# Kernel tuning notes

Measured on AMD Instinct MI355X. Metric: run time of the kernel, lower is better.

## Reference

```python
import jax, jax.numpy as jnp
import numpy as np

B, C, H, W = 16, 256, 64, 64
NUM_HEADS = 4
GROUPS = 8
EPS = 1e-5


def setup_inputs() -> dict:
    key = jax.random.key(0)
    ks = jax.random.split(key, 7)
    x = jax.random.normal(ks[0], (B, C, H, W), dtype=jnp.float32)
    # GroupNorm affine params (torch default: weight=1, bias=0; randomize slightly for a stronger test)
    norm_w = jnp.ones((C,), jnp.float32) + 0.1 * jax.random.normal(ks[1], (C,), jnp.float32)
    norm_b = 0.1 * jax.random.normal(ks[2], (C,), jnp.float32)
    # 1x1 convs == channel GEMMs; kaiming-uniform-ish init scale
    s = 1.0 / np.sqrt(C)
    qkv_w = jax.random.uniform(ks[3], (3 * C, C), jnp.float32, -s, s)
    qkv_b = jax.random.uniform(ks[4], (3 * C,), jnp.float32, -s, s)
    proj_w = jax.random.uniform(ks[5], (C, C), jnp.float32, -s, s)
    proj_b = jax.random.uniform(ks[6], (C,), jnp.float32, -s, s)
    return {"x": x, "norm_w": norm_w, "norm_b": norm_b,
            "qkv_w": qkv_w, "qkv_b": qkv_b, "proj_w": proj_w, "proj_b": proj_b}


def reference(x, norm_w, norm_b, qkv_w, qkv_b, proj_w, proj_b):
    b, c, h, w = x.shape
    nh = NUM_HEADS
    dh = c // nh
    n = h * w
    # GroupNorm(8, C)
    xg = x.reshape(b, GROUPS, c // GROUPS, h, w)
    mean = xg.mean(axis=(2, 3, 4), keepdims=True)
    var = xg.var(axis=(2, 3, 4), keepdims=True)
    xn = ((xg - mean) * jax.lax.rsqrt(var + EPS)).reshape(b, c, h, w)
    xn = xn * norm_w[None, :, None, None] + norm_b[None, :, None, None]
    # QKV 1x1 conv as channel GEMM
    qkv = jnp.einsum('bchw,oc->bohw', xn, qkv_w) + qkv_b[None, :, None, None]
    qkv = qkv.reshape(b, 3, nh, dh, n)
    q, k, v = qkv[:, 0], qkv[:, 1], qkv[:, 2]  # each (B, nh, dh, N)
    scale = dh ** (-0.5)
    # Faithful to original einsum labeling: contracts over spatial axis,
    # attention matrix is over the HEADS axis: attn (B, dh, nh, nh)
    attn = jnp.einsum('bnhd,bmhd->bhnm', q * scale, k)
    attn = jax.nn.softmax(attn, axis=-1)
    out = jnp.einsum('bhnm,bmhd->bnhd', attn, v).reshape(b, c, h, w)
    return jnp.einsum('bchw,oc->bohw', out, proj_w) + proj_b[None, :, None, None] + x
```

## Files before the change

kernel.cpp:

```cpp
#include <hip/hip_runtime.h>
#include <stdint.h>

#define BB 16
#define CC 256
#define PP 4096

typedef __attribute__((ext_vector_type(4))) float f32x4;
typedef __attribute__((ext_vector_type(8))) short bf16x8;

static __device__ __forceinline__ float bf2f(unsigned short u) {
    union { uint32_t i; float f; } w; w.i = ((uint32_t)u) << 16; return w.f;
}
static __device__ __forceinline__ unsigned short f2bf(float f) {
    union { float f; uint32_t i; } w; w.f = f;
    uint32_t u = w.i;
    uint32_t r = u + 0x7FFFu + ((u >> 16) & 1u);
    return (unsigned short)(r >> 16);
}
static __device__ __forceinline__ float dot4(f32x4 a, f32x4 b) {
    return a.x * b.x + a.y * b.y + a.z * b.z + a.w * b.w;
}

__global__ void gn_partial_k(const float* __restrict__ x, float* __restrict__ Sx,
                             float* __restrict__ Sxx) {
    int ch0 = blockIdx.x * 8;
    int t = threadIdx.x;
    int lc = t >> 5, l32 = t & 31;
    int ch = ch0 + lc;
    const f32x4* v = (const f32x4*)(x + (size_t)ch * PP);
    float s = 0.f, ss = 0.f;
    for (int i = l32; i < PP / 4; i += 32) {
        f32x4 tv = v[i];
        s  += tv.x + tv.y + tv.z + tv.w;
        ss += tv.x * tv.x + tv.y * tv.y + tv.z * tv.z + tv.w * tv.w;
    }
    for (int off = 16; off > 0; off >>= 1) {
        s  += __shfl_down(s, off, 32);
        ss += __shfl_down(ss, off, 32);
    }
    if (l32 == 0) { Sx[ch] = s; Sxx[ch] = ss; }
}

__global__ void gn_final_k(const float* __restrict__ Sx, const float* __restrict__ Sxx,
                           const float* __restrict__ nw, const float* __restrict__ nb,
                           float* __restrict__ a_s, float* __restrict__ b_s,
                           float* __restrict__ s_vec) {
    int b = blockIdx.x, c = threadIdx.x;
    __shared__ float lsx[256], lsxx[256];
    float mySx = Sx[b * CC + c];
    lsx[c] = mySx; lsxx[c] = Sxx[b * CC + c];
    __syncthreads();
    int g0 = (c >> 5) << 5;
    float S = 0.f, SS = 0.f;
    for (int j = 0; j < 32; j++) { S += lsx[g0 + j]; SS += lsxx[g0 + j]; }
    const float inv = 1.0f / 131072.0f;
    float mean = S * inv;
    float var = SS * inv - mean * mean;
    float rstd = rsqrtf(var + 1e-5f);
    float w = nw[c];
    float a = rstd * w;
    float sh = nb[c] - mean * rstd * w;
    a_s[b * CC + c] = a;
    b_s[b * CC + c] = sh;
    s_vec[b * CC + c] = a * mySx + 4096.0f * sh;
}

__global__ void cvt_bf16_k(const float* __restrict__ in, unsigned short* __restrict__ out, int n) {
    int i = blockIdx.x * 256 + threadIdx.x;
    if (i < n) out[i] = f2bf(in[i]);
}

__global__ void wvt_k(const float* __restrict__ Wv, unsigned short* __restrict__ WvT) {
    int tc1 = blockIdx.x & 3, tc2 = blockIdx.x >> 2;
    int c1_0 = tc1 * 64, c2_0 = tc2 * 64;
    __shared__ unsigned short T[64][65];
    int t = threadIdx.x;
    int r = t >> 2, q = (t & 3) * 16;
    for (int j = 0; j < 4; j++) {
        f32x4 v = *(const f32x4*)(Wv + (size_t)(c1_0 + r) * 256 + c2_0 + q + j * 4);
        T[r][q + j * 4 + 0] = f2bf(v.x);
        T[r][q + j * 4 + 1] = f2bf(v.y);
        T[r][q + j * 4 + 2] = f2bf(v.z);
        T[r][q + j * 4 + 3] = f2bf(v.w);
    }
    __syncthreads();
    union { unsigned short h[16]; uint4 u[2]; } buf;
    for (int j = 0; j < 16; j++) buf.h[j] = T[q + j][r];
    unsigned short* dst = WvT + (size_t)(c2_0 + r) * 256 + c1_0 + q;
    *(uint4*)dst       = buf.u[0];
    *(uint4*)(dst + 8) = buf.u[1];
}

__global__ void xnt_k(const float* __restrict__ x, const float* __restrict__ a_s,
                      const float* __restrict__ b_s, unsigned short* __restrict__ xnT,
                      unsigned short* __restrict__ xnC) {
    int pt = blockIdx.x & 63, ct = (blockIdx.x >> 6) & 3, b = blockIdx.x >> 8;
    int c0 = ct * 64, p0 = pt * 64;
    __shared__ unsigned short T[64][66];
    int t = threadIdx.x;
    int cl = t >> 4, pl4 = (t & 15) * 4;
    for (int i = 0; i < 4; i++) {
        int c = c0 + i * 16 + cl;
        float a = a_s[b * CC + c], sh = b_s[b * CC + c];
        f32x4 v = *(const f32x4*)(x + ((size_t)b * CC + c) * PP + p0 + pl4);
        ushort4 u;
        u.x = f2bf(a * v.x + sh);
        u.y = f2bf(a * v.y + sh);
        u.z = f2bf(a * v.z + sh);
        u.w = f2bf(a * v.w + sh);
        T[i * 16 + cl][pl4 + 0] = u.x;
        T[i * 16 + cl][pl4 + 1] = u.y;
        T[i * 16 + cl][pl4 + 2] = u.z;
        T[i * 16 + cl][pl4 + 3] = u.w;
        *(ushort4*)(xnC + ((size_t)b * CC + c) * PP + p0 + pl4) = u;
    }
    __syncthreads();
    int pl = t >> 2, c16 = (t & 3) * 16;
    union { unsigned short h[16]; uint4 u[2]; } buf;
    for (int j = 0; j < 16; j++) buf.h[j] = T[c16 + j][pl];
    unsigned short* dst = xnT + ((size_t)b * PP + p0 + pl) * CC + c0 + c16;
    *(uint4*)dst       = buf.u[0];
    *(uint4*)(dst + 8) = buf.u[1];
}

static __device__ __forceinline__ void gemm_core(const unsigned short* __restrict__ Rg,
                                                 const unsigned short* __restrict__ Cg,
                                                 int kLen, int rstride,
                                                 f32x4 (&acc)[4][4]) {
    __shared__ unsigned short Rs[128][32];
    __shared__ unsigned short Cs[128][32];
    int t = threadIdx.x;
    int lane = t & 63, wave = t >> 6;
    int wm = wave >> 1, wn = wave & 1;
    int lr = lane & 15, lq = lane >> 4;
    int srow = t >> 2;
    int ssl = ((t & 3) ^ ((t >> 3) & 3)) * 8;
    int sd  = (t & 3) * 8;
    int fsw = (lr >> 1) & 3;
    for (int mi = 0; mi < 4; mi++)
        for (int ni = 0; ni < 4; ni++) {
            acc[mi][ni][0] = 0.f; acc[mi][ni][1] = 0.f;
            acc[mi][ni][2] = 0.f; acc[mi][ni][3] = 0.f;
        }
    const unsigned short* gr0 = Rg + (size_t)srow * rstride + ssl;
    const unsigned short* gr1 = gr0 + (size_t)64 * rstride;
    const unsigned short* gc0 = Cg + (size_t)srow * rstride + ssl;
    const unsigned short* gc1 = gc0 + (size_t)64 * rstride;
    uint4 ra0 = *(const uint4*)(gr0);
    uint4 ra1 = *(const uint4*)(gr1);
    uint4 rc0 = *(const uint4*)(gc0);
    uint4 rc1 = *(const uint4*)(gc1);
    for (int k0 = 0; k0 < kLen; k0 += 32) {
        __syncthreads();
        *(uint4*)&Rs[srow][sd]      = ra0;
        *(uint4*)&Rs[srow + 64][sd] = ra1;
        *(uint4*)&Cs[srow][sd]      = rc0;
        *(uint4*)&Cs[srow + 64][sd] = rc1;
        __syncthreads();
        int kn = k0 + 32;
        if (kn < kLen) {
            ra0 = *(const uint4*)(gr0 + kn);
            ra1 = *(const uint4*)(gr1 + kn);
            rc0 = *(const uint4*)(gc0 + kn);
            rc1 = *(const uint4*)(gc1 + kn);
        }
        bf16x8 af[4], bfr[4];
        for (int mi = 0; mi < 4; mi++)
            af[mi]  = *(const bf16x8*)&Rs[wm * 64 + mi * 16 + lr][(lq ^ fsw) * 8];
        for (int ni = 0; ni < 4; ni++)
            bfr[ni] = *(const bf16x8*)&Cs[wn * 64 + ni * 16 + lr][(lq ^ fsw) * 8];
        for (int mi = 0; mi < 4; mi++)
            for (int ni = 0; ni < 4; ni++)
                acc[mi][ni] = __builtin_amdgcn_mfma_f32_16x16x32_bf16(af[mi], bfr[ni], acc[mi][ni], 0, 0, 0);
    }
}

__global__ __launch_bounds__(256, 3) void gram_k(const unsigned short* __restrict__ xnC,
                                                 float* __restrict__ Gpart) {
    int pc  = blockIdx.x & 7;
    int t12 = (blockIdx.x >> 3) & 3;
    int b   = blockIdx.x >> 5;
    int t1 = (t12 >> 1) * 128;
    int t2 = (t12 & 1) * 128;
    f32x4 acc[4][4];
    gemm_core(xnC + ((size_t)b * CC + t2) * PP + pc * 512,
              xnC + ((size_t)b * CC + t1) * PP + pc * 512, 512, PP, acc);
    int t = threadIdx.x, lane = t & 63, wave = t >> 6;
    int wm = wave >> 1, wn = wave & 1, lr = lane & 15, lq = lane >> 4;
    float* dst = Gpart + ((size_t)(pc * 16 + b)) * 65536;
    for (int mi = 0; mi < 4; mi++) {
        int c2q = t2 + wm * 64 + mi * 16 + lq * 4;
        for (int ni = 0; ni < 4; ni++) {
            int c1 = t1 + wn * 64 + ni * 16 + lr;
            *(f32x4*)(dst + (size_t)c1 * 256 + c2q) = acc[mi][ni];
        }
    }
}

__global__ void greduce_k(const float* __restrict__ Gpart, unsigned short* __restrict__ Gb) {
    int i = blockIdx.x * 256 + threadIdx.x;
    float s = 0.f;
    for (int pc = 0; pc < 8; pc++) s += Gpart[(size_t)pc * 16 * 65536 + i];
    Gb[i] = f2bf(s);
}

__global__ __launch_bounds__(256, 3) void u_gemm_k(const unsigned short* __restrict__ Gb,
                                                   const unsigned short* __restrict__ Wqkvb,
                                                   float* __restrict__ UT) {
    int t12 = blockIdx.x & 3, b = blockIdx.x >> 2;
    int t1 = (t12 >> 1) * 128;
    int t2 = (t12 & 1) * 128;
    f32x4 acc[4][4];
    gemm_core(Gb + ((size_t)b * 256 + t1) * 256,
              Wqkvb + (size_t)(256 + t2) * 256, 256, 256, acc);
    int t = threadIdx.x, lane = t & 63, wave = t >> 6;
    int wm = wave >> 1, wn = wave & 1, lr = lane & 15, lq = lane >> 4;
    for (int mi = 0; mi < 4; mi++) {
        int c1q = t1 + wm * 64 + mi * 16 + lq * 4;
        for (int ni = 0; ni < 4; ni++) {
            int kr = t2 + wn * 64 + ni * 16 + lr;
            *(f32x4*)(UT + ((size_t)b * 256 + kr) * 256 + c1q) = acc[mi][ni];
        }
    }
}

__global__ void scoresfin_k(const float* __restrict__ qkv_w, const float* __restrict__ qkv_b,
                            const float* __restrict__ UT, const float* __restrict__ s_vec,
                            float* __restrict__ attn) {
    int h = blockIdx.x & 63, b = blockIdx.x >> 6;
    int l = threadIdx.x;
    int c = l * 4;
    f32x4 sv = *(const f32x4*)(s_vec + b * CC + c);
    f32x4 wq[4], wk[4], ut[4];
    for (int n = 0; n < 4; n++) wq[n] = *(const f32x4*)(qkv_w + (size_t)(n * 64 + h) * 256 + c);
    for (int m = 0; m < 4; m++) wk[m] = *(const f32x4*)(qkv_w + (size_t)(256 + m * 64 + h) * 256 + c);
    for (int m = 0; m < 4; m++) ut[m] = *(const f32x4*)(UT + ((size_t)b * 256 + m * 64 + h) * 256 + c);
    float red[24];
    for (int n = 0; n < 4; n++)
        for (int m = 0; m < 4; m++) red[n * 4 + m] = dot4(wq[n], ut[m]);
    for (int n = 0; n < 4; n++) red[16 + n] = dot4(wq[n], sv);
    for (int m = 0; m < 4; m++) red[20 + m] = dot4(wk[m], sv);
    #pragma unroll
    for (int i = 0; i < 24; i++)
        for (int off = 32; off > 0; off >>= 1)
            red[i] += __shfl_xor(red[i], off);
    __shared__ float sred[24];
    if (l == 0)
        for (int i = 0; i < 24; i++) sred[i] = red[i];
    __syncthreads();
    if (l < 4) {
        int n = l;
        float bq = qkv_b[n * 64 + h];
        float dqn = sred[16 + n];
        float lg[4];
        for (int m = 0; m < 4; m++) {
            float bk = qkv_b[256 + m * 64 + h];
            lg[m] = 0.125f * (sred[n * 4 + m] + bq * sred[20 + m] + bk * dqn + 4096.0f * bq * bk);
        }
        float mx = fmaxf(fmaxf(lg[0], lg[1]), fmaxf(lg[2], lg[3]));
        float e0 = expf(lg[0] - mx), e1 = expf(lg[1] - mx);
        float e2 = expf(lg[2] - mx), e3 = expf(lg[3] - mx);
        float inv = 1.0f / (e0 + e1 + e2 + e3);
        float* dst = attn + ((size_t)(b * 64 + h) * 4 + n) * 4;
        dst[0] = e0 * inv; dst[1] = e1 * inv; dst[2] = e2 * inv; dst[3] = e3 * inv;
    }
}

__global__ void make_wp_k(const float* __restrict__ proj_w, const float* __restrict__ attn,
                          const float* __restrict__ qkv_b, const float* __restrict__ proj_b,
                          unsigned short* __restrict__ Wp, float* __restrict__ bias2) {
    int t = threadIdx.x;
    int o = blockIdx.x & 255, b = blockIdx.x >> 8;
    int m = t >> 6, hh = t & 63;
    float s = 0.f;
    for (int n = 0; n < 4; n++)
        s += proj_w[o * 256 + n * 64 + hh] * attn[((size_t)(b * 64 + hh) * 4 + n) * 4 + m];
    Wp[((size_t)b * 256 + o) * 256 + t] = f2bf(s);
    float contrib = s * qkv_b[512 + t];
    int lane = t & 63, wave = t >> 6;
    for (int off = 32; off > 0; off >>= 1) contrib += __shfl_down(contrib, off);
    __shared__ float red[4];
    if (lane == 0) red[wave] = contrib;
    __syncthreads();
    if (t == 0) bias2[b * 256 + o] = proj_b[o] + red[0] + red[1] + red[2] + red[3];
}

__global__ __launch_bounds__(256, 3) void make_wc_k(const unsigned short* __restrict__ WvT,
                                                    const unsigned short* __restrict__ Wp,
                                                    unsigned short* __restrict__ Wc) {
    int t12 = blockIdx.x & 3, b = blockIdx.x >> 2;
    int c20 = (t12 & 1) * 128;
    int o0  = (t12 >> 1) * 128;
    f32x4 acc[4][4];
    gemm_core(WvT + (size_t)c20 * 256, Wp + ((size_t)b * 256 + o0) * 256, 256, 256, acc);
    int t = threadIdx.x, lane = t & 63, wave = t >> 6;
    int wm = wave >> 1, wn = wave & 1, lr = lane & 15, lq = lane >> 4;
    for (int mi = 0; mi < 4; mi++) {
        int c2q = c20 + wm * 64 + mi * 16 + lq * 4;
        for (int ni = 0; ni < 4; ni++) {
            int o = o0 + wn * 64 + ni * 16 + lr;
            ushort4 u;
            u.x = f2bf(acc[mi][ni][0]);
            u.y = f2bf(acc[mi][ni][1]);
            u.z = f2bf(acc[mi][ni][2]);
            u.w = f2bf(acc[mi][ni][3]);
            *(ushort4*)(Wc + ((size_t)b * 256 + o) * 256 + c2q) = u;
        }
    }
}

__global__ __launch_bounds__(256, 3) void final_gemm_k(const unsigned short* __restrict__ Wc,
                                                       const unsigned short* __restrict__ xnT,
                                                       const float* __restrict__ bias2,
                                                       const float* __restrict__ x,
                                                       float* __restrict__ out) {
    int nt = blockIdx.x & 31;
    int rest = blockIdx.x >> 5;
    int mt = rest & 1;
    int b  = rest >> 1;
    int o0 = mt * 128, p0 = nt * 128;
    f32x4 acc[4][4];
    gemm_core(xnT + ((size_t)b * PP + p0) * 256, Wc + ((size_t)b * 256 + o0) * 256, 256, 256, acc);
    int t = threadIdx.x, lane = t & 63, wave = t >> 6;
    int wm = wave >> 1, wn = wave & 1, lr = lane & 15, lq = lane >> 4;
    for (int mi = 0; mi < 4; mi++) {
        int p4 = p0 + wm * 64 + mi * 16 + lq * 4;
        for (int ni = 0; ni < 4; ni++) {
            int o = o0 + wn * 64 + ni * 16 + lr;
            size_t idx = ((size_t)b * CC + o) * PP + p4;
            float bias = bias2[b * CC + o];
            f32x4 xv = *(const f32x4*)(x + idx);
            f32x4 r;
            r[0] = acc[mi][ni][0] + bias + xv[0];
            r[1] = acc[mi][ni][1] + bias + xv[1];
            r[2] = acc[mi][ni][2] + bias + xv[2];
            r[3] = acc[mi][ni][3] + bias + xv[3];
            *(f32x4*)(out + idx) = r;
        }
    }
}

extern "C" void kernel_launch(void* const* d_in, const int* in_sizes, int n_in,
                              void* d_out, int out_size, void* d_ws, size_t ws_size,
                              hipStream_t stream) {
    const float* x      = (const float*)d_in[0];
    const float* norm_w = (const float*)d_in[1];
    const float* norm_b = (const float*)d_in[2];
    const float* qkv_w  = (const float*)d_in[3];
    const float* qkv_b  = (const float*)d_in[4];
    const float* proj_w = (const float*)d_in[5];
    const float* proj_b = (const float*)d_in[6];
    float* out = (float*)d_out;

    char* ws = (char*)d_ws;
    size_t off = 0;
    auto alloc = [&](size_t bytes) {
        void* p = ws + off;
        off += (bytes + 255) & ~(size_t)255;
        return p;
    };
    float* Sx    = (float*)alloc(BB * CC * sizeof(float));
    float* Sxx   = (float*)alloc(BB * CC * sizeof(float));
    float* a_s   = (float*)alloc(BB * CC * sizeof(float));
    float* b_s   = (float*)alloc(BB * CC * sizeof(float));
    float* s_vec = (float*)alloc(BB * CC * sizeof(float));
    float* attn  = (float*)alloc((size_t)BB * 64 * 16 * sizeof(float));
    float* bias2 = (float*)alloc(BB * CC * sizeof(float));
    unsigned short* Wqkvb = (unsigned short*)alloc((size_t)768 * 256 * 2);
    unsigned short* WvT   = (unsigned short*)alloc((size_t)256 * 256 * 2);
    unsigned short* Wp    = (unsigned short*)alloc((size_t)BB * 65536 * 2);
    unsigned short* Wc    = (unsigned short*)alloc((size_t)BB * 65536 * 2);
    unsigned short* Gb    = (unsigned short*)alloc((size_t)BB * 65536 * 2);
    float*          UT    = (float*)alloc((size_t)BB * 65536 * 4);
    float*          Gpart = (float*)alloc((size_t)8 * BB * 65536 * 4);
    unsigned short* xnT   = (unsigned short*)alloc((size_t)BB * PP * CC * 2);
    unsigned short* xnC   = (unsigned short*)alloc((size_t)BB * PP * CC * 2);

    gn_partial_k<<<BB * CC / 8, 256, 0, stream>>>(x, Sx, Sxx);
    gn_final_k<<<BB, 256, 0, stream>>>(Sx, Sxx, norm_w, norm_b, a_s, b_s, s_vec);
    cvt_bf16_k<<<768, 256, 0, stream>>>(qkv_w, Wqkvb, 768 * 256);
    wvt_k<<<16, 256, 0, stream>>>(qkv_w + (size_t)512 * 256, WvT);
    xnt_k<<<4096, 256, 0, stream>>>(x, a_s, b_s, xnT, xnC);
    gram_k<<<BB * 4 * 8, 256, 0, stream>>>(xnC, Gpart);
    greduce_k<<<BB * 65536 / 256, 256, 0, stream>>>(Gpart, Gb);
    u_gemm_k<<<BB * 4, 256, 0, stream>>>(Gb, Wqkvb, UT);
    scoresfin_k<<<BB * 64, 64, 0, stream>>>(qkv_w, qkv_b, UT, s_vec, attn);
    make_wp_k<<<BB * 256, 256, 0, stream>>>(proj_w, attn, qkv_b, proj_b, Wp, bias2);
    make_wc_k<<<BB * 4, 256, 0, stream>>>(WvT, Wp, Wc);
    final_gemm_k<<<BB * 2 * 32, 256, 0, stream>>>(Wc, xnT, bias2, x, out);
}
```

Before: 242.2 us.

## Replace split-K gram plus reduction with single-pass 64x64 tile gram kernel

The Gram matrix kernel no longer splits the spatial reduction into eight partial fp32 slabs followed by a separate reduction kernel. Each block now computes a 64x64 output tile over the full K dimension and writes bf16 results directly. This removes the large partial-sum buffer traffic and one launch. In exchange, input rows are re-read more times, only 256 blocks run each with a long serial K loop, and the loop is sync-heavy, which can limit latency hiding.

```diff
diff --git a/kernel.cpp b/kernel.cpp
--- a/kernel.cpp
+++ b/kernel.cpp
@@ -175,33 +175,58 @@
     }
 }
 
-__global__ __launch_bounds__(256, 3) void gram_k(const unsigned short* __restrict__ xnC,
-                                                 float* __restrict__ Gpart) {
-    int pc  = blockIdx.x & 7;
-    int t12 = (blockIdx.x >> 3) & 3;
-    int b   = blockIdx.x >> 5;
-    int t1 = (t12 >> 1) * 128;
-    int t2 = (t12 & 1) * 128;
-    f32x4 acc[4][4];
-    gemm_core(xnC + ((size_t)b * CC + t2) * PP + pc * 512,
-              xnC + ((size_t)b * CC + t1) * PP + pc * 512, 512, PP, acc);
-    int t = threadIdx.x, lane = t & 63, wave = t >> 6;
-    int wm = wave >> 1, wn = wave & 1, lr = lane & 15, lq = lane >> 4;
-    float* dst = Gpart + ((size_t)(pc * 16 + b)) * 65536;
+__global__ __launch_bounds__(256) void gram64_k(const unsigned short* __restrict__ xnC,
+                                                unsigned short* __restrict__ Gb) {
+    int tile = blockIdx.x & 15, b = blockIdx.x >> 4;
+    int t1 = (tile & 3) * 64;
+    int t2 = (tile >> 2) * 64;
+    __shared__ unsigned short Rs[64][32];
+    __shared__ unsigned short Cs[64][32];
+    int t = threadIdx.x;
+    int lane = t & 63, wave = t >> 6;
+    int lr = lane & 15, lq = lane >> 4;
+    int srow = t >> 2;
+    int ssl = ((t & 3) ^ ((t >> 3) & 3)) * 8;
+    int sd  = (t & 3) * 8;
+    int fsw = (lr >> 1) & 3;
+    f32x4 acc[4];
     for (int mi = 0; mi < 4; mi++) {
-        int c2q = t2 + wm * 64 + mi * 16 + lq * 4;
-        for (int ni = 0; ni < 4; ni++) {
-            int c1 = t1 + wn * 64 + ni * 16 + lr;
-            *(f32x4*)(dst + (size_t)c1 * 256 + c2q) = acc[mi][ni];
-        }
-    }
-}
-
-__global__ void greduce_k(const float* __restrict__ Gpart, unsigned short* __restrict__ Gb) {
-    int i = blockIdx.x * 256 + threadIdx.x;
-    float s = 0.f;
-    for (int pc = 0; pc < 8; pc++) s += Gpart[(size_t)pc * 16 * 65536 + i];
-    Gb[i] = f2bf(s);
+        acc[mi][0] = 0.f; acc[mi][1] = 0.f; acc[mi][2] = 0.f; acc[mi][3] = 0.f;
+    }
+    const unsigned short* grp = xnC + ((size_t)b * CC + t2 + srow) * PP + ssl;
+    const unsigned short* gcp = xnC + ((size_t)b * CC + t1 + srow) * PP + ssl;
+    uint4 ra = *(const uint4*)(grp);
+    uint4 rc = *(const uint4*)(gcp);
+    uint4 rb = *(const uint4*)(grp + 32);
+    uint4 rd = *(const uint4*)(gcp + 32);
+    for (int k0 = 0; k0 < PP; k0 += 32) {
+        __syncthreads();
+        *(uint4*)&Rs[srow][sd] = ra;
+        *(uint4*)&Cs[srow][sd] = rc;
+        ra = rb; rc = rd;
+        int kn = k0 + 64;
+        if (kn < PP) {
+            rb = *(const uint4*)(grp + kn);
+            rd = *(const uint4*)(gcp + kn);
+        }
+        __syncthreads();
+        bf16x8 af[4];
+        for (int mi = 0; mi < 4; mi++)
+            af[mi] = *(const bf16x8*)&Rs[mi * 16 + lr][(lq ^ fsw) * 8];
+        bf16x8 bfr = *(const bf16x8*)&Cs[wave * 16 + lr][(lq ^ fsw) * 8];
+        for (int mi = 0; mi < 4; mi++)
+            acc[mi] = __builtin_amdgcn_mfma_f32_16x16x32_bf16(af[mi], bfr, acc[mi], 0, 0, 0);
+    }
+    int c1 = t1 + wave * 16 + lr;
+    for (int mi = 0; mi < 4; mi++) {
+        int c2q = t2 + mi * 16 + lq * 4;
+        ushort4 u;
+        u.x = f2bf(acc[mi][0]);
+        u.y = f2bf(acc[mi][1]);
+        u.z = f2bf(acc[mi][2]);
+        u.w = f2bf(acc[mi][3]);
+        *(ushort4*)(Gb + ((size_t)b * 256 + c1) * 256 + c2q) = u;
+    }
 }
 
 __global__ __launch_bounds__(256, 3) void u_gemm_k(const unsigned short* __restrict__ Gb,
@@ -372,7 +397,6 @@
     unsigned short* Wc    = (unsigned short*)alloc((size_t)BB * 65536 * 2);
     unsigned short* Gb    = (unsigned short*)alloc((size_t)BB * 65536 * 2);
     float*          UT    = (float*)alloc((size_t)BB * 65536 * 4);
-    float*          Gpart = (float*)alloc((size_t)8 * BB * 65536 * 4);
     unsigned short* xnT   = (unsigned short*)alloc((size_t)BB * PP * CC * 2);
     unsigned short* xnC   = (unsigned short*)alloc((size_t)BB * PP * CC * 2);
 
@@ -381,8 +405,7 @@
     cvt_bf16_k<<<768, 256, 0, stream>>>(qkv_w, Wqkvb, 768 * 256);
     wvt_k<<<16, 256, 0, stream>>>(qkv_w + (size_t)512 * 256, WvT);
     xnt_k<<<4096, 256, 0, stream>>>(x, a_s, b_s, xnT, xnC);
-    gram_k<<<BB * 4 * 8, 256, 0, stream>>>(xnC, Gpart);
-    greduce_k<<<BB * 65536 / 256, 256, 0, stream>>>(Gpart, Gb);
+    gram64_k<<<BB * 16, 256, 0, stream>>>(xnC, Gb);
     u_gemm_k<<<BB * 4, 256, 0, stream>>>(Gb, Wqkvb, UT);
     scoresfin_k<<<BB * 64, 64, 0, stream>>>(qkv_w, qkv_b, UT, s_vec, attn);
     make_wp_k<<<BB * 256, 256, 0, stream>>>(proj_w, attn, qkv_b, proj_b, Wp, bias2);
```

After: 250.6 us. 1.03x slower.
